# Performance work log

Measured on AMD Instinct MI355X. Metric: run time of the kernel, lower is better.

Reference implementation:

```python
import jax, jax.numpy as jnp
import numpy as np

HEADS = 4
HEAD_DIM = 32
NUM_GRAPHS = 512


def _transformer_conv(x, Wq, bq, Wk, bk, Wv, bv, Ws, bs, src, dst):
    # PyG TransformerConv, concat=False, root_weight=True, beta=False, eval mode (no dropout).
    N = x.shape[0]
    q = (x @ Wq + bq).reshape(N, HEADS, HEAD_DIM)
    k = (x @ Wk + bk).reshape(N, HEADS, HEAD_DIM)
    v = (x @ Wv + bv).reshape(N, HEADS, HEAD_DIM)
    scale = 1.0 / np.sqrt(HEAD_DIM).astype(np.float32)
    # per-edge attention logits: query at target (dst), key at source (src)
    logits = jnp.einsum('ehd,ehd->eh', q[dst], k[src]) * scale  # [E, H]
    # segment softmax over incoming edges of each target node
    m = jax.ops.segment_max(logits, dst, num_segments=N)        # [N, H]
    p = jnp.exp(logits - m[dst])                                # [E, H]
    denom = jax.ops.segment_sum(p, dst, num_segments=N)         # [N, H]
    a = p / jnp.maximum(denom[dst], 1e-16)                      # [E, H]
    msg = a[:, :, None] * v[src]                                # [E, H, D]
    out = jax.ops.segment_sum(msg, dst, num_segments=N)         # [N, H, D]
    out = out.mean(axis=1)                                      # concat=False -> head mean
    return out + (x @ Ws + bs)                                  # root/skip connection


def _global_mean_pool(x, batch, num_graphs):
    s = jax.ops.segment_sum(x, batch, num_segments=num_graphs)
    cnt = jax.ops.segment_sum(jnp.ones((x.shape[0],), x.dtype), batch, num_segments=num_graphs)
    return s / jnp.maximum(cnt, 1.0)[:, None]


def setup_inputs() -> dict:
    key = jax.random.key(0)
    ks = jax.random.split(key, 20)
    N, E, C, H = 100000, 1600000, 128, 32
    d = {
        'x': jax.random.normal(ks[0], (N, C), jnp.float32),
        'edge_index': jax.random.randint(ks[1], (2, E), 0, N, jnp.int64),
        'batch': jnp.sort(jax.random.randint(ks[2], (N,), 0, NUM_GRAPHS, jnp.int64)),
    }
    def lin(k, fan_in, fan_out):
        lim = 1.0 / np.sqrt(fan_in)
        k1, k2 = jax.random.split(k)
        return (jax.random.uniform(k1, (fan_in, fan_out), jnp.float32, -lim, lim),
                jax.random.uniform(k2, (fan_out,), jnp.float32, -lim, lim))
    d['Wq1'], d['bq1'] = lin(ks[3], C, HEADS * HEAD_DIM)
    d['Wk1'], d['bk1'] = lin(ks[4], C, HEADS * HEAD_DIM)
    d['Wv1'], d['bv1'] = lin(ks[5], C, HEADS * HEAD_DIM)
    d['Ws1'], d['bs1'] = lin(ks[6], C, H)
    d['Wq2'], d['bq2'] = lin(ks[7], H, HEADS * HEAD_DIM)
    d['Wk2'], d['bk2'] = lin(ks[8], H, HEADS * HEAD_DIM)
    d['Wv2'], d['bv2'] = lin(ks[9], H, HEADS * HEAD_DIM)
    d['Ws2'], d['bs2'] = lin(ks[10], H, H)
    return d


def reference(x, edge_index, batch, Wq1, bq1, Wk1, bk1, Wv1, bv1, Ws1, bs1,
              Wq2, bq2, Wk2, bk2, Wv2, bv2, Ws2, bs2):
    src, dst = edge_index[0], edge_index[1]
    h = _transformer_conv(x, Wq1, bq1, Wk1, bk1, Wv1, bv1, Ws1, bs1, src, dst)
    h = jax.nn.relu(h)
    h = _transformer_conv(h, Wq2, bq2, Wk2, bk2, Wv2, bv2, Ws2, bs2, src, dst)
    h = jax.nn.relu(h)
    return _global_mean_pool(h, batch, NUM_GRAPHS)
```

## Files before the change

### kernel.cpp

```cpp
#include <hip/hip_runtime.h>
#include <math.h>

typedef __attribute__((ext_vector_type(8))) short bf16x8;
typedef __attribute__((ext_vector_type(4))) float f32x4;

__device__ __forceinline__ float b2f(unsigned short u) {
    union { unsigned u32; float f; } x; x.u32 = (unsigned)u << 16; return x.f;
}
__device__ __forceinline__ unsigned short f2b(float f) {
    union { float f; unsigned u32; } x; x.f = f;
    unsigned u = x.u32;
    unsigned r = (u + 0x7fffu + ((u >> 16) & 1u)) >> 16;
    return (unsigned short)r;
}

__device__ __forceinline__ f32x4 mfma16(bf16x8 a, bf16x8 b, f32x4 c) {
    return __builtin_amdgcn_mfma_f32_16x16x32_bf16(a, b, c, 0, 0, 0);
}

__device__ __forceinline__ void async_copy16(const unsigned* g, void* l) {
    __builtin_amdgcn_global_load_lds(
        (const __attribute__((address_space(1))) unsigned*)g,
        (__attribute__((address_space(3))) unsigned*)l, 16, 0, 0);
}


__global__ __launch_bounds__(256) void hist_k(const int* __restrict__ dst, int* __restrict__ deg, int E) {
    int e = blockIdx.x * 256 + threadIdx.x;
    if (e < E) atomicAdd(&deg[dst[e]], 1);
}

__global__ __launch_bounds__(256) void scanA_k(const int* __restrict__ deg, int* __restrict__ rowptr,
                                               int* __restrict__ partials, int N) {
    __shared__ int sh[256];
    int t = threadIdx.x;
    int base = blockIdx.x * 1024 + t * 4;
    int v0 = 0, v1 = 0, v2 = 0, v3 = 0;
    if (base + 0 < N) v0 = deg[base + 0];
    if (base + 1 < N) v1 = deg[base + 1];
    if (base + 2 < N) v2 = deg[base + 2];
    if (base + 3 < N) v3 = deg[base + 3];
    sh[t] = v0 + v1 + v2 + v3;
    __syncthreads();
    for (int off = 1; off < 256; off <<= 1) {
        int add = (t >= off) ? sh[t - off] : 0;
        __syncthreads();
        sh[t] += add;
        __syncthreads();
    }
    int run = (t > 0) ? sh[t - 1] : 0;
    if (base + 0 < N) rowptr[base + 0] = run; run += v0;
    if (base + 1 < N) rowptr[base + 1] = run; run += v1;
    if (base + 2 < N) rowptr[base + 2] = run; run += v2;
    if (base + 3 < N) rowptr[base + 3] = run;
    if (t == 255) partials[blockIdx.x] = sh[255];
}

__global__ void scanB_k(int* partials, int nch) {
    if (threadIdx.x == 0 && blockIdx.x == 0) {
        int run = 0;
        for (int i = 0; i < nch; ++i) { int x = partials[i]; partials[i] = run; run += x; }
        partials[nch] = run;
    }
}

__global__ __launch_bounds__(256) void addoff_k(int* __restrict__ rowptr, const int* __restrict__ partials,
                                                int N, int nch) {
    int t = threadIdx.x;
    int off = partials[blockIdx.x];
    int base = blockIdx.x * 1024;
    for (int i = 0; i < 4; ++i) {
        int idx = base + t + i * 256;
        if (idx < N) rowptr[idx] += off;
    }
    if (blockIdx.x == 0 && t == 0) rowptr[N] = partials[nch];
}

__global__ __launch_bounds__(256) void scatter_k(const int* __restrict__ src, const int* __restrict__ dst,
                                                 const int* __restrict__ rowptr, int* __restrict__ cnt,
                                                 int* __restrict__ srcid, int E) {
    int e = blockIdx.x * 256 + threadIdx.x;
    if (e < E) {
        int d = dst[e];
        int pos = rowptr[d] + atomicAdd(&cnt[d], 1);
        srcid[pos] = src[e];
    }
}


__global__ __launch_bounds__(256) void cvt_k(const float* __restrict__ x,
                                             unsigned short* __restrict__ hi,
                                             unsigned short* __restrict__ lo, long n4) {
    long stride = (long)gridDim.x * 256;
    for (long i = (long)blockIdx.x * 256 + threadIdx.x; i < n4; i += stride) {
        float4 v = ((const float4*)x)[i];
        ushort4 h, L;
        h.x = f2b(v.x); L.x = f2b(v.x - b2f(h.x));
        h.y = f2b(v.y); L.y = f2b(v.y - b2f(h.y));
        h.z = f2b(v.z); L.z = f2b(v.z - b2f(h.z));
        h.w = f2b(v.w); L.w = f2b(v.w - b2f(h.w));
        ((ushort4*)hi)[i] = h;
        ((ushort4*)lo)[i] = L;
    }
}


__global__ __launch_bounds__(256) void wprep_k(
    const float* __restrict__ Wq, const float* __restrict__ Wk,
    const float* __restrict__ Wv, const float* __restrict__ Ws,
    int ksteps, unsigned* __restrict__ fhi, unsigned* __restrict__ flo)
{
    int idx = blockIdx.x * 256 + threadIdx.x;
    int total = 26 * ksteps * 64 * 4;
    if (idx >= total) return;
    int w = idx & 3;
    int lane = (idx >> 2) & 63;
    int tmp = idx >> 8;
    int kk = tmp % ksteps;
    int t = tmp / ksteps;
    int col = t * 16 + (lane & 15);
    int k0 = kk * 32 + ((lane >> 4) << 3) + (w << 1);
    const float* W; int ow, c;
    if (col < 128)      { W = Wq; ow = 128; c = col; }
    else if (col < 256) { W = Wk; ow = 128; c = col - 128; }
    else if (col < 384) { W = Wv; ow = 128; c = col - 256; }
    else                { W = Ws; ow = 32;  c = col - 384; }
    float v0 = W[(size_t)k0 * ow + c];
    float v1 = W[(size_t)(k0 + 1) * ow + c];
    unsigned short h0 = f2b(v0), h1 = f2b(v1);
    unsigned short l0 = f2b(v0 - b2f(h0)), l1 = f2b(v1 - b2f(h1));
    fhi[idx] = (unsigned)h0 | ((unsigned)h1 << 16);
    flo[idx] = (unsigned)l0 | ((unsigned)l1 << 16);
}


template<int KSTEPS>
__global__ __launch_bounds__(256, 3) void qkvs_mfma(const unsigned short* __restrict__ Xhi,
    const unsigned short* __restrict__ Xlo, int Cin, int N,
    const unsigned* __restrict__ fhi, const unsigned* __restrict__ flo,
    const float* __restrict__ bq, const float* __restrict__ bk,
    const float* __restrict__ bv, const float* __restrict__ bs,
    float* __restrict__ q, unsigned short* __restrict__ kb,
    unsigned short* __restrict__ vb, float* __restrict__ sk)
{
    constexpr int NT = 13;
    __shared__ float4 ldsB[2 * 2 * NT * 64];

    int tid = threadIdx.x;
    int lane = tid & 63, wv = tid >> 6;
    int r0 = (blockIdx.x * 4 + wv) * 16;
    int tbase = blockIdx.y * NT;

    int row = r0 + (lane & 15);
    int rowc = row < N ? row : N - 1;
    const int asub = (lane >> 4) << 3;

    for (int t = wv; t < NT; t += 4) {
        size_t srcoff = (((size_t)(tbase + t) * KSTEPS + 0) * 64 + lane) * 4;
        async_copy16(fhi + srcoff, &ldsB[(0 * 2 + 0) * NT * 64 + t * 64]);
        async_copy16(flo + srcoff, &ldsB[(0 * 2 + 1) * NT * 64 + t * 64]);
    }
    bf16x8 ah = *(const bf16x8*)(Xhi + (size_t)rowc * Cin + asub);
    bf16x8 al = *(const bf16x8*)(Xlo + (size_t)rowc * Cin + asub);

    f32x4 acc[NT];
#pragma unroll
    for (int t = 0; t < NT; ++t) acc[t] = (f32x4){0.f, 0.f, 0.f, 0.f};

#pragma unroll
    for (int kk = 0; kk < KSTEPS; ++kk) {
        __syncthreads();
        bf16x8 ahn, aln;
        if (kk + 1 < KSTEPS) {
            int nbuf = (kk + 1) & 1;
            for (int t = wv; t < NT; t += 4) {
                size_t srcoff = (((size_t)(tbase + t) * KSTEPS + kk + 1) * 64 + lane) * 4;
                async_copy16(fhi + srcoff, &ldsB[(nbuf * 2 + 0) * NT * 64 + t * 64]);
                async_copy16(flo + srcoff, &ldsB[(nbuf * 2 + 1) * NT * 64 + t * 64]);
            }
            size_t aoff = (size_t)rowc * Cin + (kk + 1) * 32 + asub;
            ahn = *(const bf16x8*)(Xhi + aoff);
            aln = *(const bf16x8*)(Xlo + aoff);
        }
        const float4* base = &ldsB[(kk & 1) * 2 * NT * 64];
#pragma unroll
        for (int t = 0; t < NT; ++t) {
            bf16x8 bh = *(const bf16x8*)&base[t * 64 + lane];
            bf16x8 bl = *(const bf16x8*)&base[NT * 64 + t * 64 + lane];
            acc[t] = mfma16(ah, bh, acc[t]);
            acc[t] = mfma16(al, bh, acc[t]);
            acc[t] = mfma16(ah, bl, acc[t]);
        }
        if (kk + 1 < KSTEPS) { ah = ahn; al = aln; }
    }

#pragma unroll
    for (int t = 0; t < NT; ++t) {
        int col = (tbase + t) * 16 + (lane & 15);
        int sel; const float* bp; int c;
        if (col < 128)      { sel = 0; bp = bq; c = col; }
        else if (col < 256) { sel = 1; bp = bk; c = col - 128; }
        else if (col < 384) { sel = 2; bp = bv; c = col - 256; }
        else                { sel = 3; bp = bs; c = col - 384; }
        float bias = bp[c];
#pragma unroll
        for (int r = 0; r < 4; ++r) {
            int orow = r0 + ((lane >> 4) << 2) + r;
            if (orow >= N) continue;
            float val = acc[t][r] + bias;
            if (sel == 0)      q [(size_t)orow * 128 + c] = val;
            else if (sel == 1) kb[(size_t)orow * 128 + c] = f2b(val);
            else if (sel == 2) vb[(size_t)orow * 128 + c] = f2b(val);
            else               sk[(size_t)orow * 32  + c] = val;
        }
    }
}


__global__ __launch_bounds__(256) void attn_k(const float* __restrict__ q,
    const unsigned short* __restrict__ k, const unsigned short* __restrict__ v,
    const float* __restrict__ sk,
    const int* __restrict__ rowptr, const int* __restrict__ srcid,
    float* __restrict__ outF, unsigned short* __restrict__ outHi,
    unsigned short* __restrict__ outLo, int mode, int N)
{
    int grp = threadIdx.x >> 5;
    int n = blockIdx.x * 8 + grp;
    if (n >= N) return;
    int l = threadIdx.x & 31;
    int s = l & 7;
    const float scale = 0.17677669529663687f;

    float4 qv = *(const float4*)(q + (size_t)n * 128 + l * 4);
    float4 acc = make_float4(0.f, 0.f, 0.f, 0.f);
    float m = -INFINITY, lsum = 0.f;

    int e0 = rowptr[n], e1 = rowptr[n + 1];
    if (e0 < e1) {
        int sID = srcid[e0];
        ushort4 kcur = *(const ushort4*)(k + (size_t)sID * 128 + l * 4);
        ushort4 vcur = *(const ushort4*)(v + (size_t)sID * 128 + l * 4);
        for (int e = e0; e < e1; ++e) {
            int nextS = (e + 1 < e1) ? srcid[e + 1] : sID;
            ushort4 kn = *(const ushort4*)(k + (size_t)nextS * 128 + l * 4);
            ushort4 vn = *(const ushort4*)(v + (size_t)nextS * 128 + l * 4);
            float p = qv.x * b2f(kcur.x) + qv.y * b2f(kcur.y)
                    + qv.z * b2f(kcur.z) + qv.w * b2f(kcur.w);
            p += __shfl_xor(p, 1, 8);
            p += __shfl_xor(p, 2, 8);
            p += __shfl_xor(p, 4, 8);
            float logit = p * scale;
            float mn = fmaxf(m, logit);
            float ex = __expf(logit - mn);
            float sc = __expf(m - mn);
            lsum = lsum * sc + ex;
            acc.x = acc.x * sc + ex * b2f(vcur.x);
            acc.y = acc.y * sc + ex * b2f(vcur.y);
            acc.z = acc.z * sc + ex * b2f(vcur.z);
            acc.w = acc.w * sc + ex * b2f(vcur.w);
            m = mn;
            kcur = kn; vcur = vn;
        }
    }

    float inv = 0.25f / fmaxf(lsum, 1e-16f);
    float rx = acc.x * inv, ry = acc.y * inv, rz = acc.z * inv, rw = acc.w * inv;
    rx += __shfl_xor(rx, 8, 32);  rx += __shfl_xor(rx, 16, 32);
    ry += __shfl_xor(ry, 8, 32);  ry += __shfl_xor(ry, 16, 32);
    rz += __shfl_xor(rz, 8, 32);  rz += __shfl_xor(rz, 16, 32);
    rw += __shfl_xor(rw, 8, 32);  rw += __shfl_xor(rw, 16, 32);

    if (l < 8) {
        const float* skp = sk + (size_t)n * 32 + s * 4;
        float o0 = fmaxf(rx + skp[0], 0.f), o1 = fmaxf(ry + skp[1], 0.f);
        float o2 = fmaxf(rz + skp[2], 0.f), o3 = fmaxf(rw + skp[3], 0.f);
        if (mode == 0) {
            *(float4*)(outF + (size_t)n * 32 + s * 4) = make_float4(o0, o1, o2, o3);
        } else {
            ushort4 h, L;
            h.x = f2b(o0); L.x = f2b(o0 - b2f(h.x));
            h.y = f2b(o1); L.y = f2b(o1 - b2f(h.y));
            h.z = f2b(o2); L.z = f2b(o2 - b2f(h.z));
            h.w = f2b(o3); L.w = f2b(o3 - b2f(h.w));
            *(ushort4*)(outHi + (size_t)n * 32 + s * 4) = h;
            *(ushort4*)(outLo + (size_t)n * 32 + s * 4) = L;
        }
    }
}


__global__ __launch_bounds__(256) void pool_k(const float* __restrict__ h, const int* __restrict__ batch,
                                              float* __restrict__ out, int N)
{
    int g = blockIdx.x;
    int t = threadIdx.x;
    int lo = 0, hi = N;
    while (lo < hi) { int mid = (lo + hi) >> 1; if (batch[mid] < g) lo = mid + 1; else hi = mid; }
    int start = lo;
    lo = 0; hi = N;
    while (lo < hi) { int mid = (lo + hi) >> 1; if (batch[mid] < g + 1) lo = mid + 1; else hi = mid; }
    int end = lo;
    int c = t & 31, r0 = t >> 5;
    float s = 0.f;
    for (int r = start + r0; r < end; r += 8) s += h[(size_t)r * 32 + c];
    __shared__ float sh[256];
    sh[t] = s;
    __syncthreads();
    if (t < 32) {
        float tot = sh[t] + sh[t + 32] + sh[t + 64] + sh[t + 96]
                  + sh[t + 128] + sh[t + 160] + sh[t + 192] + sh[t + 224];
        float cnt = (float)(end - start);
        out[(size_t)g * 32 + t] = tot / fmaxf(cnt, 1.f);
    }
}


extern "C" void kernel_launch(void* const* d_in, const int* in_sizes, int n_in,
                              void* d_out, int out_size, void* d_ws, size_t ws_size,
                              hipStream_t stream) {
    const float* x   = (const float*)d_in[0];
    const int* ei    = (const int*)d_in[1];
    const int* batch = (const int*)d_in[2];
    const float *Wq1 = (const float*)d_in[3],  *bq1 = (const float*)d_in[4];
    const float *Wk1 = (const float*)d_in[5],  *bk1 = (const float*)d_in[6];
    const float *Wv1 = (const float*)d_in[7],  *bv1 = (const float*)d_in[8];
    const float *Ws1 = (const float*)d_in[9],  *bs1 = (const float*)d_in[10];
    const float *Wq2 = (const float*)d_in[11], *bq2 = (const float*)d_in[12];
    const float *Wk2 = (const float*)d_in[13], *bk2 = (const float*)d_in[14];
    const float *Wv2 = (const float*)d_in[15], *bv2 = (const float*)d_in[16];
    const float *Ws2 = (const float*)d_in[17], *bs2 = (const float*)d_in[18];
    float* out = (float*)d_out;

    int N = in_sizes[0] / 128;
    int E = in_sizes[1] / 2;
    const int* src = ei;
    const int* dst = ei + E;

    char* ws = (char*)d_ws;
    size_t off = 0;
    auto alloc = [&](size_t bytes) -> void* {
        void* p = ws + off;
        off += (bytes + 255) & ~(size_t)255;
        return p;
    };
    int* deg      = (int*)alloc((size_t)N * 4);
    int* cnt      = (int*)alloc((size_t)N * 4);
    int* rowptr   = (int*)alloc(((size_t)N + 1) * 4);
    int* partials = (int*)alloc(4096);
    int* srcid    = (int*)alloc((size_t)E * 4);
    unsigned* fhi1 = (unsigned*)alloc(26 * 4 * 64 * 4 * 4);
    unsigned* flo1 = (unsigned*)alloc(26 * 4 * 64 * 4 * 4);
    unsigned* fhi2 = (unsigned*)alloc(26 * 1 * 64 * 4 * 4);
    unsigned* flo2 = (unsigned*)alloc(26 * 1 * 64 * 4 * 4);
    unsigned short* Xhi = (unsigned short*)alloc((size_t)N * 128 * 2);
    unsigned short* Xlo = (unsigned short*)alloc((size_t)N * 128 * 2);
    float* q            = (float*)alloc((size_t)N * 128 * 4);
    unsigned short* kb  = (unsigned short*)alloc((size_t)N * 128 * 2);
    unsigned short* vb  = (unsigned short*)alloc((size_t)N * 128 * 2);
    float* sk     = (float*)alloc((size_t)N * 32 * 4);
    unsigned short* h1hi = (unsigned short*)alloc((size_t)N * 32 * 2);
    unsigned short* h1lo = (unsigned short*)alloc((size_t)N * 32 * 2);
    float* h2     = (float*)alloc((size_t)N * 32 * 4);

    hipMemsetAsync(deg, 0, (size_t)N * 4, stream);
    hipMemsetAsync(cnt, 0, (size_t)N * 4, stream);

    int nch = (N + 1023) / 1024;
    hist_k<<<(E + 255) / 256, 256, 0, stream>>>(dst, deg, E);
    scanA_k<<<nch, 256, 0, stream>>>(deg, rowptr, partials, N);
    scanB_k<<<1, 64, 0, stream>>>(partials, nch);
    addoff_k<<<nch, 256, 0, stream>>>(rowptr, partials, N, nch);
    scatter_k<<<(E + 255) / 256, 256, 0, stream>>>(src, dst, rowptr, cnt, srcid, E);

    wprep_k<<<(26 * 4 * 64 * 4 + 255) / 256, 256, 0, stream>>>(Wq1, Wk1, Wv1, Ws1, 4, fhi1, flo1);
    wprep_k<<<(26 * 1 * 64 * 4 + 255) / 256, 256, 0, stream>>>(Wq2, Wk2, Wv2, Ws2, 1, fhi2, flo2);
    cvt_k<<<2048, 256, 0, stream>>>(x, Xhi, Xlo, (long)N * 32);

    dim3 gq((N + 63) / 64, 2);
    qkvs_mfma<4><<<gq, 256, 0, stream>>>(Xhi, Xlo, 128, N, fhi1, flo1,
        bq1, bk1, bv1, bs1, q, kb, vb, sk);
    attn_k<<<(N + 7) / 8, 256, 0, stream>>>(q, kb, vb, sk, rowptr, srcid,
        nullptr, h1hi, h1lo, 1, N);
    qkvs_mfma<1><<<gq, 256, 0, stream>>>(h1hi, h1lo, 32, N, fhi2, flo2,
        bq2, bk2, bv2, bs2, q, kb, vb, sk);
    attn_k<<<(N + 7) / 8, 256, 0, stream>>>(q, kb, vb, sk, rowptr, srcid,
        h2, nullptr, nullptr, 0, N);
    pool_k<<<512, 256, 0, stream>>>(h2, batch, out, N);
}
```

Before: 592.5 us.

## Make QKVS GEMM persistent with full weight slice resident in LDS

The projection GEMM now launches a fixed grid of 128x2 blocks of 1024 threads. Each block loads its entire column slice of split-bf16 weights for all K steps into LDS once, then its 16 waves loop over row tiles. This removes the per-k double-buffered weight reloads and the barriers that each small block needed. The cost is fewer blocks (256 on a large-CU device), 1024-thread blocks with possible register pressure from launch bounds, and a serial row loop per wave.

```diff
diff --git a/kernel.cpp b/kernel.cpp
--- a/kernel.cpp
+++ b/kernel.cpp
@@ -135,83 +135,89 @@
 
 
 template<int KSTEPS>
-__global__ __launch_bounds__(256, 3) void qkvs_mfma(const unsigned short* __restrict__ Xhi,
+__global__ __launch_bounds__(1024) void qkvs_mfma(const unsigned short* __restrict__ Xhi,
     const unsigned short* __restrict__ Xlo, int Cin, int N,
     const unsigned* __restrict__ fhi, const unsigned* __restrict__ flo,
     const float* __restrict__ bq, const float* __restrict__ bk,
     const float* __restrict__ bv, const float* __restrict__ bs,
     float* __restrict__ q, unsigned short* __restrict__ kb,
-    unsigned short* __restrict__ vb, float* __restrict__ sk)
+    unsigned short* __restrict__ vb, float* __restrict__ sk, int rtPer)
 {
     constexpr int NT = 13;
-    __shared__ float4 ldsB[2 * 2 * NT * 64];
+    constexpr int NIDX = KSTEPS * NT * 2 * 64;
+    __shared__ float4 ldsB[NIDX];
 
     int tid = threadIdx.x;
-    int lane = tid & 63, wv = tid >> 6;
-    int r0 = (blockIdx.x * 4 + wv) * 16;
+    int lane = tid & 63, wid = tid >> 6;
     int tbase = blockIdx.y * NT;
 
-    int row = r0 + (lane & 15);
-    int rowc = row < N ? row : N - 1;
+    for (int u = tid; u < NIDX; u += 1024) {
+        int l = u & 63;
+        int rest = u >> 6;
+        int plane = rest & 1;
+        int tt = (rest >> 1) % NT;
+        int kk = (rest >> 1) / NT;
+        const unsigned* srcp = plane ? flo : fhi;
+        size_t so = (((size_t)(tbase + tt) * KSTEPS + kk) * 64 + l) * 4;
+        async_copy16(srcp + so, &ldsB[u - l]);
+    }
+    __syncthreads();
+
     const int asub = (lane >> 4) << 3;
-
-    for (int t = wv; t < NT; t += 4) {
-        size_t srcoff = (((size_t)(tbase + t) * KSTEPS + 0) * 64 + lane) * 4;
-        async_copy16(fhi + srcoff, &ldsB[(0 * 2 + 0) * NT * 64 + t * 64]);
-        async_copy16(flo + srcoff, &ldsB[(0 * 2 + 1) * NT * 64 + t * 64]);
-    }
-    bf16x8 ah = *(const bf16x8*)(Xhi + (size_t)rowc * Cin + asub);
-    bf16x8 al = *(const bf16x8*)(Xlo + (size_t)rowc * Cin + asub);
-
-    f32x4 acc[NT];
-#pragma unroll
-    for (int t = 0; t < NT; ++t) acc[t] = (f32x4){0.f, 0.f, 0.f, 0.f};
-
-#pragma unroll
-    for (int kk = 0; kk < KSTEPS; ++kk) {
-        __syncthreads();
-        bf16x8 ahn, aln;
-        if (kk + 1 < KSTEPS) {
-            int nbuf = (kk + 1) & 1;
-            for (int t = wv; t < NT; t += 4) {
-                size_t srcoff = (((size_t)(tbase + t) * KSTEPS + kk + 1) * 64 + lane) * 4;
-                async_copy16(fhi + srcoff, &ldsB[(nbuf * 2 + 0) * NT * 64 + t * 64]);
-                async_copy16(flo + srcoff, &ldsB[(nbuf * 2 + 1) * NT * 64 + t * 64]);
+    int rtTotal = (N + 15) >> 4;
+    int rtStart = blockIdx.x * rtPer;
+    int rtEnd = rtStart + rtPer; if (rtEnd > rtTotal) rtEnd = rtTotal;
+
+    for (int rt = rtStart + wid; rt < rtEnd; rt += 16) {
+        int row = rt * 16 + (lane & 15);
+        int rowc = row < N ? row : N - 1;
+        const unsigned short* xh = Xhi + (size_t)rowc * Cin + asub;
+        const unsigned short* xl = Xlo + (size_t)rowc * Cin + asub;
+
+        f32x4 acc[NT];
+#pragma unroll
+        for (int t = 0; t < NT; ++t) acc[t] = (f32x4){0.f, 0.f, 0.f, 0.f};
+
+        bf16x8 ah = *(const bf16x8*)xh;
+        bf16x8 al = *(const bf16x8*)xl;
+#pragma unroll
+        for (int kk = 0; kk < KSTEPS; ++kk) {
+            bf16x8 ahn, aln;
+            if (kk + 1 < KSTEPS) {
+                ahn = *(const bf16x8*)(xh + (kk + 1) * 32);
+                aln = *(const bf16x8*)(xl + (kk + 1) * 32);
             }
-            size_t aoff = (size_t)rowc * Cin + (kk + 1) * 32 + asub;
-            ahn = *(const bf16x8*)(Xhi + aoff);
-            aln = *(const bf16x8*)(Xlo + aoff);
+            const float4* base = &ldsB[kk * NT * 2 * 64];
+#pragma unroll
+            for (int t = 0; t < NT; ++t) {
+                bf16x8 bh = *(const bf16x8*)&base[(t * 2 + 0) * 64 + lane];
+                bf16x8 bl = *(const bf16x8*)&base[(t * 2 + 1) * 64 + lane];
+                acc[t] = mfma16(ah, bh, acc[t]);
+                acc[t] = mfma16(al, bh, acc[t]);
+                acc[t] = mfma16(ah, bl, acc[t]);
+            }
+            if (kk + 1 < KSTEPS) { ah = ahn; al = aln; }
         }
-        const float4* base = &ldsB[(kk & 1) * 2 * NT * 64];
+
 #pragma unroll
         for (int t = 0; t < NT; ++t) {
-            bf16x8 bh = *(const bf16x8*)&base[t * 64 + lane];
-            bf16x8 bl = *(const bf16x8*)&base[NT * 64 + t * 64 + lane];
-            acc[t] = mfma16(ah, bh, acc[t]);
-            acc[t] = mfma16(al, bh, acc[t]);
-            acc[t] = mfma16(ah, bl, acc[t]);
-        }
-        if (kk + 1 < KSTEPS) { ah = ahn; al = aln; }
-    }
-
-#pragma unroll
-    for (int t = 0; t < NT; ++t) {
-        int col = (tbase + t) * 16 + (lane & 15);
-        int sel; const float* bp; int c;
-        if (col < 128)      { sel = 0; bp = bq; c = col; }
-        else if (col < 256) { sel = 1; bp = bk; c = col - 128; }
-        else if (col < 384) { sel = 2; bp = bv; c = col - 256; }
-        else                { sel = 3; bp = bs; c = col - 384; }
-        float bias = bp[c];
-#pragma unroll
-        for (int r = 0; r < 4; ++r) {
-            int orow = r0 + ((lane >> 4) << 2) + r;
-            if (orow >= N) continue;
-            float val = acc[t][r] + bias;
-            if (sel == 0)      q [(size_t)orow * 128 + c] = val;
-            else if (sel == 1) kb[(size_t)orow * 128 + c] = f2b(val);
-            else if (sel == 2) vb[(size_t)orow * 128 + c] = f2b(val);
-            else               sk[(size_t)orow * 32  + c] = val;
+            int col = (tbase + t) * 16 + (lane & 15);
+            int sel; const float* bp; int c;
+            if (col < 128)      { sel = 0; bp = bq; c = col; }
+            else if (col < 256) { sel = 1; bp = bk; c = col - 128; }
+            else if (col < 384) { sel = 2; bp = bv; c = col - 256; }
+            else                { sel = 3; bp = bs; c = col - 384; }
+            float bias = bp[c];
+#pragma unroll
+            for (int r = 0; r < 4; ++r) {
+                int orow = rt * 16 + ((lane >> 4) << 2) + r;
+                if (orow >= N) continue;
+                float val = acc[t][r] + bias;
+                if (sel == 0)      q [(size_t)orow * 128 + c] = val;
+                else if (sel == 1) kb[(size_t)orow * 128 + c] = f2b(val);
+                else if (sel == 2) vb[(size_t)orow * 128 + c] = f2b(val);
+                else               sk[(size_t)orow * 32  + c] = val;
+            }
         }
     }
 }
@@ -376,13 +382,15 @@
     wprep_k<<<(26 * 1 * 64 * 4 + 255) / 256, 256, 0, stream>>>(Wq2, Wk2, Wv2, Ws2, 1, fhi2, flo2);
     cvt_k<<<2048, 256, 0, stream>>>(x, Xhi, Xlo, (long)N * 32);
 
-    dim3 gq((N + 63) / 64, 2);
-    qkvs_mfma<4><<<gq, 256, 0, stream>>>(Xhi, Xlo, 128, N, fhi1, flo1,
-        bq1, bk1, bv1, bs1, q, kb, vb, sk);
+    int rtTotal = (N + 15) / 16;
+    int rtPer = (rtTotal + 127) / 128;
+    dim3 gq(128, 2);
+    qkvs_mfma<4><<<gq, 1024, 0, stream>>>(Xhi, Xlo, 128, N, fhi1, flo1,
+        bq1, bk1, bv1, bs1, q, kb, vb, sk, rtPer);
     attn_k<<<(N + 7) / 8, 256, 0, stream>>>(q, kb, vb, sk, rowptr, srcid,
         nullptr, h1hi, h1lo, 1, N);
-    qkvs_mfma<1><<<gq, 256, 0, stream>>>(h1hi, h1lo, 32, N, fhi2, flo2,
-        bq2, bk2, bv2, bs2, q, kb, vb, sk);
+    qkvs_mfma<1><<<gq, 1024, 0, stream>>>(h1hi, h1lo, 32, N, fhi2, flo2,
+        bq2, bk2, bv2, bs2, q, kb, vb, sk, rtPer);
     attn_k<<<(N + 7) / 8, 256, 0, stream>>>(q, kb, vb, sk, rowptr, srcid,
         h2, nullptr, nullptr, 0, N);
     pool_k<<<512, 256, 0, stream>>>(h2, batch, out, N);
```

After: 567.5 us. 4.2% less time.
